# Kernel tuning notes

Hardware: AMD Instinct MI355X
Metric: run time of the kernel (lower is better)

Reference implementation:

```python
import jax, jax.numpy as jnp
import numpy as np

KEY_DIM = 1024
SCALE = KEY_DIM ** -0.5


def setup_inputs() -> dict:
    key = jax.random.key(0)
    k1, k2, k3, k4 = jax.random.split(key, 4)
    B, S, E = 4, 2048, 1024
    x = jax.random.normal(k1, (B, S, E), dtype=jnp.float32)
    WQ = jax.random.normal(k2, (KEY_DIM, E), dtype=jnp.float32) * (E ** -0.5)
    WK = jax.random.normal(k3, (KEY_DIM, E), dtype=jnp.float32) * (E ** -0.5)
    WV = jax.random.normal(k4, (KEY_DIM, E), dtype=jnp.float32) * (E ** -0.5)
    return {"x": x, "WQ": WQ, "WK": WK, "WV": WV}


def reference(x, WQ, WK, WV):
    # x: [B, S, E]; Linear(bias=False) weights are [out, in] as in torch.
    q = jnp.einsum('bse,ke->bsk', x, WQ)   # [B, S, K]
    k = jnp.einsum('bse,ke->bsk', x, WK)   # [B, S, K]
    v = jnp.einsum('bse,ve->bsv', x, WV)   # [B, S, V]
    scores = jnp.einsum('bsk,btk->bst', q, k) * SCALE  # [B, S, S]
    # Faithful to torch: mask where tril(scores) == 0 (upper triangle).
    masked = jnp.where(jnp.tril(scores) == 0, -jnp.inf, scores)
    attn = jax.nn.softmax(masked, axis=-1)
    return jnp.einsum('bst,btv->bsv', attn, v)  # dropout=0.0 -> identity
```

## Files before the change

### kernel.cpp

```cpp
#include <hip/hip_runtime.h>

typedef _Float16 f16x8 __attribute__((ext_vector_type(8)));
typedef unsigned short u16x8v __attribute__((ext_vector_type(8)));
typedef unsigned short u16x4v __attribute__((ext_vector_type(4)));
typedef float f32x4 __attribute__((ext_vector_type(4)));

constexpr int SEQ = 2048;
constexpr int DIM = 1024;
constexpr int BATCH = 4;
constexpr size_t NBS = (size_t)BATCH * SEQ * DIM;

static __device__ __forceinline__ unsigned short f2h(float f) {
    return __builtin_bit_cast(unsigned short, (_Float16)f);
}
static __device__ __forceinline__ float h2f(unsigned short u) {
    return (float)__builtin_bit_cast(_Float16, u);
}
static __device__ __forceinline__ f16x8 ldsld(const unsigned short* p) {
    return __builtin_bit_cast(f16x8, *(const u16x8v*)p);
}
static __device__ __forceinline__ void gld_lds16(const unsigned short* g, unsigned short* l) {
    __builtin_amdgcn_global_load_lds(
        (const __attribute__((address_space(1))) void*)g,
        (__attribute__((address_space(3))) void*)l, 16, 0, 0);
}

__global__ __launch_bounds__(256) void cvt_all(
    const float* __restrict__ X,
    const float* __restrict__ W0, const float* __restrict__ W1,
    const float* __restrict__ W2,
    unsigned short* __restrict__ Xf, unsigned short* __restrict__ Wf)
{
    const int b = blockIdx.x;
    const float* src;
    unsigned short* dst;
    int i;
    if (b < 8192) {
        src = X; dst = Xf;
        i = b * 256 + threadIdx.x;
    } else {
        const int wb = b - 8192;
        const int z = wb >> 10;
        src = (z == 0) ? W0 : (z == 1) ? W1 : W2;
        dst = Wf + (size_t)z * DIM * DIM;
        i = (wb & 1023) * 256 + threadIdx.x;
    }
    float4 f = ((const float4*)src)[i];
    u16x4v h;
    h.x = f2h(f.x); h.y = f2h(f.y); h.z = f2h(f.z); h.w = f2h(f.w);
    ((u16x4v*)dst)[i] = h;
}

__global__ __launch_bounds__(256) void qkv_gemm(
    const unsigned short* __restrict__ Xf, const unsigned short* __restrict__ Wf,
    unsigned short* __restrict__ Qf, unsigned short* __restrict__ Kf,
    unsigned short* __restrict__ Vt)
{
    __shared__ __attribute__((aligned(16))) unsigned short Ah[128 * 64];
    __shared__ __attribute__((aligned(16))) unsigned short Bh[128 * 64];
    const int m0 = blockIdx.x * 128, n0 = blockIdx.y * 128, z = blockIdx.z;
    const unsigned short* Wz = Wf + (size_t)z * DIM * DIM;
    const int tid = threadIdx.x;
    const int w = tid >> 6, lane = tid & 63, q = lane >> 4, c = lane & 15;
    const int wrow = (w >> 1) * 64, wcol = (w & 1) * 64;
    const int g8 = lane >> 3;
    const int cu = (lane & 7) ^ g8;
    const int srow = w * 8 + g8;
    const int scol = cu * 8;
    unsigned short* lA = Ah + w * 512;
    unsigned short* lB = Bh + w * 512;
    const int c7 = c & 7;

    f32x4 acc[4][4];
#pragma unroll
    for (int a = 0; a < 4; ++a)
#pragma unroll
        for (int b = 0; b < 4; ++b) acc[a][b] = (f32x4){0.f, 0.f, 0.f, 0.f};

    for (int k0 = 0; k0 < DIM; k0 += 64) {
        __syncthreads();
        {
            const size_t ga = (size_t)(m0 + srow) * DIM + k0 + scol;
            const size_t gb = (size_t)(n0 + srow) * DIM + k0 + scol;
#pragma unroll
            for (int j = 0; j < 4; ++j) {
                gld_lds16(Xf + ga + (size_t)(j * 32) * DIM, lA + j * 2048);
                gld_lds16(Wz + gb + (size_t)(j * 32) * DIM, lB + j * 2048);
            }
        }
        __syncthreads();
#pragma unroll
        for (int kk = 0; kk < 2; ++kk) {
            f16x8 ah[4], bh[4];
#pragma unroll
            for (int mi = 0; mi < 4; ++mi)
                ah[mi] = ldsld(Ah + (wrow + mi * 16 + c) * 64 + (((kk << 2) + q) ^ c7) * 8);
#pragma unroll
            for (int ni = 0; ni < 4; ++ni)
                bh[ni] = ldsld(Bh + (wcol + ni * 16 + c) * 64 + (((kk << 2) + q) ^ c7) * 8);
#pragma unroll
            for (int mi = 0; mi < 4; ++mi)
#pragma unroll
                for (int ni = 0; ni < 4; ++ni)
                    acc[mi][ni] = __builtin_amdgcn_mfma_f32_16x16x32_f16(ah[mi], bh[ni], acc[mi][ni], 0, 0, 0);
        }
    }

    if (z == 2) {
#pragma unroll
        for (int mi = 0; mi < 4; ++mi) {
            const int mg = m0 + wrow + mi * 16 + q * 4;
            const int bb = mg >> 11, ss = mg & (SEQ - 1);
#pragma unroll
            for (int ni = 0; ni < 4; ++ni) {
                const int col = n0 + wcol + ni * 16 + c;
                u16x4v v;
                v.x = f2h(acc[mi][ni][0]);
                v.y = f2h(acc[mi][ni][1]);
                v.z = f2h(acc[mi][ni][2]);
                v.w = f2h(acc[mi][ni][3]);
                *(u16x4v*)(Vt + ((size_t)bb * DIM + col) * SEQ + ss) = v;
            }
        }
    } else {
        unsigned short* OH = z ? Kf : Qf;
#pragma unroll
        for (int mi = 0; mi < 4; ++mi)
#pragma unroll
            for (int ni = 0; ni < 4; ++ni) {
                const int col = n0 + wcol + ni * 16 + c;
#pragma unroll
                for (int r = 0; r < 4; ++r) {
                    const int row = m0 + wrow + mi * 16 + q * 4 + r;
                    OH[(size_t)row * DIM + col] = f2h(acc[mi][ni][r]);
                }
            }
    }
}

__global__ __launch_bounds__(256) void scores_gemm1b(
    const unsigned short* __restrict__ Q, const unsigned short* __restrict__ K,
    unsigned short* __restrict__ S)
{
    __shared__ __attribute__((aligned(16))) unsigned short Ah[128 * 64];
    __shared__ __attribute__((aligned(16))) unsigned short Bh[128 * 64];
    const int t = blockIdx.x;
    int ti = (int)((__builtin_sqrtf(8.f * t + 1.f) - 1.f) * 0.5f);
    while ((ti + 1) * (ti + 2) / 2 <= t) ++ti;
    while (ti * (ti + 1) / 2 > t) --ti;
    const int tj = t - ti * (ti + 1) / 2;
    const int i0 = ti * 128, j0 = tj * 128, b = blockIdx.z;
    const unsigned short* Qb = Q + (size_t)b * SEQ * DIM;
    const unsigned short* Kb = K + (size_t)b * SEQ * DIM;
    unsigned short* Sb = S + (size_t)b * SEQ * SEQ;
    const int tid = threadIdx.x;
    const int w = tid >> 6, lane = tid & 63, q = lane >> 4, c = lane & 15;
    const int wrow = (w >> 1) * 64, wcol = (w & 1) * 64;
    const int g8 = lane >> 3;
    const int cu = (lane & 7) ^ g8;
    const int srow = w * 8 + g8;
    const int scol = cu * 8;
    unsigned short* lA = Ah + w * 512;
    unsigned short* lB = Bh + w * 512;
    const int c7 = c & 7;

    f32x4 acc[4][4];
#pragma unroll
    for (int a = 0; a < 4; ++a)
#pragma unroll
        for (int bq = 0; bq < 4; ++bq) acc[a][bq] = (f32x4){0.f, 0.f, 0.f, 0.f};

    for (int k0 = 0; k0 < DIM; k0 += 64) {
        __syncthreads();
        {
            const size_t ga = (size_t)(i0 + srow) * DIM + k0 + scol;
            const size_t gb = (size_t)(j0 + srow) * DIM + k0 + scol;
#pragma unroll
            for (int j = 0; j < 4; ++j) {
                gld_lds16(Qb + ga + (size_t)(j * 32) * DIM, lA + j * 2048);
                gld_lds16(Kb + gb + (size_t)(j * 32) * DIM, lB + j * 2048);
            }
        }
        __syncthreads();
#pragma unroll
        for (int kk = 0; kk < 2; ++kk) {
            f16x8 ah[4], bh[4];
#pragma unroll
            for (int mi = 0; mi < 4; ++mi)
                ah[mi] = ldsld(Ah + (wrow + mi * 16 + c) * 64 + (((kk << 2) + q) ^ c7) * 8);
#pragma unroll
            for (int ni = 0; ni < 4; ++ni)
                bh[ni] = ldsld(Bh + (wcol + ni * 16 + c) * 64 + (((kk << 2) + q) ^ c7) * 8);
#pragma unroll
            for (int mi = 0; mi < 4; ++mi)
#pragma unroll
                for (int ni = 0; ni < 4; ++ni)
                    acc[mi][ni] = __builtin_amdgcn_mfma_f32_16x16x32_f16(ah[mi], bh[ni], acc[mi][ni], 0, 0, 0);
        }
    }
#pragma unroll
    for (int mi = 0; mi < 4; ++mi)
#pragma unroll
        for (int ni = 0; ni < 4; ++ni) {
            const int col = j0 + wcol + ni * 16 + c;
#pragma unroll
            for (int r = 0; r < 4; ++r) {
                const int row = i0 + wrow + mi * 16 + q * 4 + r;
                const float sc = acc[mi][ni][r] * 0.03125f;
                Sb[(size_t)row * SEQ + col] =
                    (sc == 0.f) ? (unsigned short)0xFC00u : f2h(sc);
            }
        }
}

__global__ __launch_bounds__(256) void softmax_row_b(
    const unsigned short* __restrict__ S, unsigned short* __restrict__ P)
{
    const int i = blockIdx.x, t = threadIdx.x;
    const size_t ro = ((size_t)blockIdx.y * SEQ + i) * SEQ;
    const int wid = t >> 6, lane = t & 63;
    __shared__ float redm[4], reds[4];
    const int j0 = t * 8;
    const int rti = (i & ~127) + 128;
    float sv[8];
    float mx = -__builtin_inff();
    if (j0 <= i) {
        u16x8v raw = *(const u16x8v*)(S + ro + j0);
#pragma unroll
        for (int u = 0; u < 8; ++u) {
            float s = (j0 + u <= i) ? h2f(raw[u]) : -__builtin_inff();
            sv[u] = s;
            mx = fmaxf(mx, s);
        }
    } else {
#pragma unroll
        for (int u = 0; u < 8; ++u) sv[u] = -__builtin_inff();
    }
#pragma unroll
    for (int off = 1; off < 64; off <<= 1) mx = fmaxf(mx, __shfl_xor(mx, off));
    if (lane == 0) redm[wid] = mx;
    __syncthreads();
    const float M = fmaxf(fmaxf(redm[0], redm[1]), fmaxf(redm[2], redm[3]));
    float sum = 0.f;
#pragma unroll
    for (int u = 0; u < 8; ++u) {
        float e = __expf(sv[u] - M);
        sv[u] = e;
        sum += e;
    }
#pragma unroll
    for (int off = 1; off < 64; off <<= 1) sum += __shfl_xor(sum, off);
    if (lane == 0) reds[wid] = sum;
    __syncthreads();
    const float rinv = 1.f / (reds[0] + reds[1] + reds[2] + reds[3]);
    if (j0 < rti) {
        u16x8v o;
#pragma unroll
        for (int u = 0; u < 8; ++u) o[u] = f2h(sv[u] * rinv);
        *(u16x8v*)(P + ro + j0) = o;
    }
}

__global__ __launch_bounds__(256) void pv_gemm(
    const unsigned short* __restrict__ Pm, const unsigned short* __restrict__ Vt,
    float* __restrict__ Out)
{
    __shared__ __attribute__((aligned(16))) unsigned short Ps[128 * 64];
    __shared__ __attribute__((aligned(16))) unsigned short Vs[128 * 64];
    const int b = blockIdx.z;
    const int i0t = (b < 2) ? blockIdx.x : 15 - blockIdx.x;
    const int i0 = i0t * 128, d0 = blockIdx.y * 128;
    const int tid = threadIdx.x;
    const int w = tid >> 6, lane = tid & 63, q = lane >> 4, c = lane & 15;
    const int wrow = (w >> 1) * 64, wcol = (w & 1) * 64;
    const int g8 = lane >> 3;
    const int cu = (lane & 7) ^ g8;
    const int srow = w * 8 + g8;
    const int scol = cu * 8;
    unsigned short* lA = Ps + w * 512;
    unsigned short* lB = Vs + w * 512;
    const int c7 = c & 7;

    f32x4 acc[4][4];
#pragma unroll
    for (int a = 0; a < 4; ++a)
#pragma unroll
        for (int bq = 0; bq < 4; ++bq) acc[a][bq] = (f32x4){0.f, 0.f, 0.f, 0.f};

    const int njs = 2 * i0t + 2;

    for (int ks = 0; ks < njs; ++ks) {
        const int j0 = ks * 64;
        __syncthreads();
        {
            const size_t gpa = ((size_t)b * SEQ + i0 + srow) * SEQ + j0 + scol;
            const size_t gva = ((size_t)b * DIM + d0 + srow) * SEQ + j0 + scol;
#pragma unroll
            for (int j = 0; j < 4; ++j) {
                gld_lds16(Pm + gpa + (size_t)(j * 32) * SEQ, lA + j * 2048);
                gld_lds16(Vt + gva + (size_t)(j * 32) * SEQ, lB + j * 2048);
            }
        }
        __syncthreads();
#pragma unroll
        for (int kk = 0; kk < 2; ++kk) {
            f16x8 ah[4], bh[4];
#pragma unroll
            for (int mi = 0; mi < 4; ++mi)
                ah[mi] = ldsld(Ps + (wrow + mi * 16 + c) * 64 + (((kk << 2) + q) ^ c7) * 8);
#pragma unroll
            for (int ni = 0; ni < 4; ++ni)
                bh[ni] = ldsld(Vs + (wcol + ni * 16 + c) * 64 + (((kk << 2) + q) ^ c7) * 8);
#pragma unroll
            for (int mi = 0; mi < 4; ++mi)
#pragma unroll
                for (int ni = 0; ni < 4; ++ni)
                    acc[mi][ni] = __builtin_amdgcn_mfma_f32_16x16x32_f16(ah[mi], bh[ni], acc[mi][ni], 0, 0, 0);
        }
    }
#pragma unroll
    for (int mi = 0; mi < 4; ++mi)
#pragma unroll
        for (int ni = 0; ni < 4; ++ni) {
            const int dcol = d0 + wcol + ni * 16 + c;
#pragma unroll
            for (int r = 0; r < 4; ++r) {
                const int i = i0 + wrow + mi * 16 + q * 4 + r;
                Out[((size_t)b * SEQ + i) * DIM + dcol] = acc[mi][ni][r];
            }
        }
}

extern "C" void kernel_launch(void* const* d_in, const int* in_sizes, int n_in,
                              void* d_out, int out_size, void* d_ws, size_t ws_size,
                              hipStream_t stream)
{
    (void)out_size; (void)ws_size;
    const float* X = nullptr;
    const float* Wv[3] = {nullptr, nullptr, nullptr};
    int nw = 0;
    for (int i = 0; i < n_in; ++i) {
        if (in_sizes[i] == (int)NBS)
            X = (const float*)d_in[i];
        else if (nw < 3)
            Wv[nw++] = (const float*)d_in[i];
    }

    unsigned short* ws = (unsigned short*)d_ws;
    unsigned short* Qf = ws;
    unsigned short* Kf = ws + NBS;
    unsigned short* Vt = ws + 2 * NBS;
    unsigned short* Xf = ws + 3 * NBS;
    unsigned short* Pp = ws + 3 * NBS;
    unsigned short* Sb = ws + 5 * NBS;
    unsigned short* Wf = ws + 7 * NBS;
    float* Out = (float*)d_out;

    cvt_all<<<dim3(8192 + 3072), 256, 0, stream>>>(X, Wv[0], Wv[1], Wv[2], Xf, Wf);

    qkv_gemm<<<dim3(64, 8, 3), 256, 0, stream>>>(Xf, Wf, Qf, Kf, Vt);

    scores_gemm1b<<<dim3(136, 1, BATCH), 256, 0, stream>>>(Qf, Kf, Sb);
    softmax_row_b<<<dim3(SEQ, BATCH), 256, 0, stream>>>(Sb, Pp);

    pv_gemm<<<dim3(16, 8, BATCH), 256, 0, stream>>>(Pp, Vt, Out);
}
```

Baseline: 245.9 us.

## Reassociate scores as X·(WQᵀWK)·Xᵀ to drop one projection GEMM

```diff
diff --git a/kernel.cpp b/kernel.cpp
--- a/kernel.cpp
+++ b/kernel.cpp
@@ -25,41 +25,108 @@
         (__attribute__((address_space(3))) void*)l, 16, 0, 0);
 }
 
-__global__ __launch_bounds__(256) void cvt_all(
+__global__ __launch_bounds__(256) void cvt_mt(
     const float* __restrict__ X,
-    const float* __restrict__ W0, const float* __restrict__ W1,
-    const float* __restrict__ W2,
-    unsigned short* __restrict__ Xf, unsigned short* __restrict__ Wf)
-{
+    const float* __restrict__ Wq32, const float* __restrict__ Wk32,
+    const float* __restrict__ Wv32,
+    unsigned short* __restrict__ Xf, unsigned short* __restrict__ Wvf,
+    unsigned short* __restrict__ Mt)
+{
+    __shared__ __attribute__((aligned(16))) unsigned short LA[128 * 64];
+    __shared__ __attribute__((aligned(16))) unsigned short LB[128 * 64];
     const int b = blockIdx.x;
-    const float* src;
-    unsigned short* dst;
-    int i;
-    if (b < 8192) {
-        src = X; dst = Xf;
-        i = b * 256 + threadIdx.x;
-    } else {
-        const int wb = b - 8192;
-        const int z = wb >> 10;
-        src = (z == 0) ? W0 : (z == 1) ? W1 : W2;
-        dst = Wf + (size_t)z * DIM * DIM;
-        i = (wb & 1023) * 256 + threadIdx.x;
-    }
-    float4 f = ((const float4*)src)[i];
-    u16x4v h;
-    h.x = f2h(f.x); h.y = f2h(f.y); h.z = f2h(f.z); h.w = f2h(f.w);
-    ((u16x4v*)dst)[i] = h;
-}
-
-__global__ __launch_bounds__(256) void qkv_gemm(
-    const unsigned short* __restrict__ Xf, const unsigned short* __restrict__ Wf,
-    unsigned short* __restrict__ Qf, unsigned short* __restrict__ Kf,
-    unsigned short* __restrict__ Vt)
+    const int tid = threadIdx.x;
+
+    if (b >= 64) {
+        const float* src;
+        unsigned short* dst;
+        int i;
+        const int cb = b - 64;
+        if (cb < 8192) {
+            src = X; dst = Xf;
+            i = cb * 256 + tid;
+        } else {
+            src = Wv32; dst = Wvf;
+            i = (cb - 8192) * 256 + tid;
+        }
+        float4 f = ((const float4*)src)[i];
+        u16x4v h;
+        h.x = f2h(f.x); h.y = f2h(f.y); h.z = f2h(f.z); h.w = f2h(f.w);
+        ((u16x4v*)dst)[i] = h;
+        return;
+    }
+
+    const int e0p = (b >> 3) * 128;
+    const int e0  = (b & 7) * 128;
+    const int w = tid >> 6, lane = tid & 63, q = lane >> 4, c = lane & 15;
+    const int wrow = (w >> 1) * 64, wcol = (w & 1) * 64;
+    const int kr = tid >> 5;
+    const int ec = (tid & 31) * 4;
+
+    f32x4 acc[4][4];
+#pragma unroll
+    for (int a = 0; a < 4; ++a)
+#pragma unroll
+        for (int bq = 0; bq < 4; ++bq) acc[a][bq] = (f32x4){0.f, 0.f, 0.f, 0.f};
+
+    for (int k0 = 0; k0 < DIM; k0 += 64) {
+        __syncthreads();
+#pragma unroll
+        for (int s = 0; s < 8; ++s) {
+            const int k = k0 + kr + 8 * s;
+            float4 av = *(const float4*)(Wk32 + (size_t)k * DIM + e0p + ec);
+            float4 bv = *(const float4*)(Wq32 + (size_t)k * DIM + e0 + ec);
+#pragma unroll
+            for (int i = 0; i < 4; ++i) {
+                const int ea = ec + i;
+                const int off = ea * 64 + (((s + ea) & 7) << 3) + kr;
+                LA[off] = f2h(((const float*)&av)[i]);
+                LB[off] = f2h(((const float*)&bv)[i]);
+            }
+        }
+        __syncthreads();
+#pragma unroll
+        for (int kk = 0; kk < 2; ++kk) {
+            f16x8 af[4], bf[4];
+#pragma unroll
+            for (int mi = 0; mi < 4; ++mi) {
+                const int ep = wrow + mi * 16 + c;
+                af[mi] = ldsld(LA + ep * 64 + (((((kk << 2) + q) + ep) & 7) << 3));
+            }
+#pragma unroll
+            for (int ni = 0; ni < 4; ++ni) {
+                const int ee = wcol + ni * 16 + c;
+                bf[ni] = ldsld(LB + ee * 64 + (((((kk << 2) + q) + ee) & 7) << 3));
+            }
+#pragma unroll
+            for (int mi = 0; mi < 4; ++mi)
+#pragma unroll
+                for (int ni = 0; ni < 4; ++ni)
+                    acc[mi][ni] = __builtin_amdgcn_mfma_f32_16x16x32_f16(af[mi], bf[ni], acc[mi][ni], 0, 0, 0);
+        }
+    }
+#pragma unroll
+    for (int mi = 0; mi < 4; ++mi)
+#pragma unroll
+        for (int ni = 0; ni < 4; ++ni) {
+            const int col = e0 + wcol + ni * 16 + c;
+#pragma unroll
+            for (int r = 0; r < 4; ++r) {
+                const int row = e0p + wrow + mi * 16 + q * 4 + r;
+                Mt[(size_t)row * DIM + col] = f2h(acc[mi][ni][r]);
+            }
+        }
+}
+
+__global__ __launch_bounds__(256) void yv_gemm(
+    const unsigned short* __restrict__ Xf, const unsigned short* __restrict__ Mt,
+    const unsigned short* __restrict__ Wvf,
+    unsigned short* __restrict__ Yf, unsigned short* __restrict__ Vt)
 {
     __shared__ __attribute__((aligned(16))) unsigned short Ah[128 * 64];
     __shared__ __attribute__((aligned(16))) unsigned short Bh[128 * 64];
     const int m0 = blockIdx.x * 128, n0 = blockIdx.y * 128, z = blockIdx.z;
-    const unsigned short* Wz = Wf + (size_t)z * DIM * DIM;
+    const unsigned short* Wz = z ? Wvf : Mt;
     const int tid = threadIdx.x;
     const int w = tid >> 6, lane = tid & 63, q = lane >> 4, c = lane & 15;
     const int wrow = (w >> 1) * 64, wcol = (w & 1) * 64;
@@ -106,7 +173,7 @@
         }
     }
 
-    if (z == 2) {
+    if (z == 1) {
 #pragma unroll
         for (int mi = 0; mi < 4; ++mi) {
             const int mg = m0 + wrow + mi * 16 + q * 4;
@@ -123,7 +190,6 @@
             }
         }
     } else {
-        unsigned short* OH = z ? Kf : Qf;
 #pragma unroll
         for (int mi = 0; mi < 4; ++mi)
 #pragma unroll
@@ -132,7 +198,7 @@
 #pragma unroll
                 for (int r = 0; r < 4; ++r) {
                     const int row = m0 + wrow + mi * 16 + q * 4 + r;
-                    OH[(size_t)row * DIM + col] = f2h(acc[mi][ni][r]);
+                    Yf[(size_t)row * DIM + col] = f2h(acc[mi][ni][r]);
                 }
             }
     }
@@ -347,20 +413,21 @@
     }
 
     unsigned short* ws = (unsigned short*)d_ws;
-    unsigned short* Qf = ws;
-    unsigned short* Kf = ws + NBS;
+    unsigned short* Yf = ws;
     unsigned short* Vt = ws + 2 * NBS;
     unsigned short* Xf = ws + 3 * NBS;
     unsigned short* Pp = ws + 3 * NBS;
     unsigned short* Sb = ws + 5 * NBS;
-    unsigned short* Wf = ws + 7 * NBS;
+    unsigned short* Wvf = ws + 7 * NBS;
+    unsigned short* Mtb = Wvf + (size_t)DIM * DIM;
     float* Out = (float*)d_out;
 
-    cvt_all<<<dim3(8192 + 3072), 256, 0, stream>>>(X, Wv[0], Wv[1], Wv[2], Xf, Wf);
-
-    qkv_gemm<<<dim3(64, 8, 3), 256, 0, stream>>>(Xf, Wf, Qf, Kf, Vt);
-
-    scores_gemm1b<<<dim3(136, 1, BATCH), 256, 0, stream>>>(Qf, Kf, Sb);
+    cvt_mt<<<dim3(64 + 8192 + 1024), 256, 0, stream>>>(
+        X, Wv[0], Wv[1], Wv[2], Xf, Wvf, Mtb);
+
+    yv_gemm<<<dim3(64, 8, 2), 256, 0, stream>>>(Xf, Mtb, Wvf, Yf, Vt);
+
+    scores_gemm1b<<<dim3(136, 1, BATCH), 256, 0, stream>>>(Yf, Xf, Sb);
     softmax_row_b<<<dim3(SEQ, BATCH), 256, 0, stream>>>(Sb, Pp);
 
     pv_gemm<<<dim3(16, 8, BATCH), 256, 0, stream>>>(Pp, Vt, Out);
```

Result: slower. 297.7 us (+21.1%).
